# Kernel optimization log

Hardware: AMD Instinct MI355X
Metric: run time of the kernel (lower is better)

## Reference

```python
import jax, jax.numpy as jnp
import numpy as np
import math

H = 16          # n_head
N_EMBD = 1024
EPS = 1e-5      # torch LayerNorm default


def setup_inputs() -> dict:
    key = jax.random.key(0)
    ks = jax.random.split(key, 6)
    B, T, C = 2, 2048, 1024
    x = jax.random.normal(ks[0], (B, T, C), dtype=jnp.float32)
    s = 0.02  # GPT-2 style init scale keeps softmax logits sane
    Wq = jax.random.normal(ks[1], (C, N_EMBD), dtype=jnp.float32) * s
    Wk = jax.random.normal(ks[2], (C, N_EMBD), dtype=jnp.float32) * s
    Wv = jax.random.normal(ks[3], (C, N_EMBD), dtype=jnp.float32) * s
    Wo = jax.random.normal(ks[4], (N_EMBD, C), dtype=jnp.float32) * s
    return {
        "x": x,
        "Wq": Wq, "bq": jnp.zeros((N_EMBD,), jnp.float32),
        "Wk": Wk, "bk": jnp.zeros((N_EMBD,), jnp.float32),
        "Wv": Wv, "bv": jnp.zeros((N_EMBD,), jnp.float32),
        "Wo": Wo, "bo": jnp.zeros((C,), jnp.float32),
        "gamma": jnp.ones((C,), jnp.float32),
        "beta": jnp.zeros((C,), jnp.float32),
    }


def reference(x, Wq, bq, Wk, bk, Wv, bv, Wo, bo, gamma, beta):
    B, T, _ = x.shape
    Dh = N_EMBD // H
    # projections -> (B, H, T, Dh)
    def split_heads(y):
        return y.reshape(B, T, H, Dh).transpose(0, 2, 1, 3)
    q = split_heads(x @ Wq + bq)
    k = split_heads(x @ Wk + bk)
    v = split_heads(x @ Wv + bv)
    # naive causal attention: explicit (B,H,T,T) scores
    att = jnp.einsum("bhtd,bhsd->bhts", q, k) * (1.0 / math.sqrt(Dh))
    causal = jnp.tril(jnp.ones((T, T), dtype=bool))
    att = jnp.where(causal[None, None], att, -jnp.inf)
    att = jax.nn.softmax(att, axis=-1)
    o = jnp.einsum("bhts,bhsd->bhtd", att, v)
    o = o.transpose(0, 2, 1, 3).reshape(B, T, N_EMBD)
    y = o @ Wo + bo
    # LayerNorm (dropout is identity at p=0 / eval)
    mu = jnp.mean(y, axis=-1, keepdims=True)
    var = jnp.var(y, axis=-1, keepdims=True)
    return (y - mu) * jax.lax.rsqrt(var + EPS) * gamma + beta
```

## Files before the change

### kernel.cpp

```cpp
#include <hip/hip_runtime.h>
#include <stdint.h>
#include <stddef.h>

typedef __attribute__((ext_vector_type(8))) short short8;
typedef __attribute__((ext_vector_type(4))) float f32x4;
typedef __attribute__((ext_vector_type(16))) float f32x16;
typedef __attribute__((ext_vector_type(4))) unsigned short us4;
typedef __attribute__((ext_vector_type(4))) unsigned u32x4;

#define DEVI static __device__ __forceinline__

DEVI unsigned short f2bf(float f) {
  unsigned u = __builtin_bit_cast(unsigned, f);
  u += 0x7FFFu + ((u >> 16) & 1u);
  return (unsigned short)(u >> 16);
}

DEVI float bf2f(unsigned short u) {
  return __builtin_bit_cast(float, ((unsigned)u) << 16);
}

DEVI f32x4 mfma16(short8 a, short8 b, f32x4 c) {
  return __builtin_amdgcn_mfma_f32_16x16x32_bf16(a, b, c, 0, 0, 0);
}

DEVI f32x16 mfma32(short8 a, short8 b, f32x16 c) {
  return __builtin_amdgcn_mfma_f32_32x32x16_bf16(a, b, c, 0, 0, 0);
}

DEVI unsigned cvtpk(float lo, float hi) {
  unsigned r;
  asm("v_cvt_pk_bf16_f32 %0, %1, %2" : "=v"(r) : "v"(lo), "v"(hi));
  return r;
}

DEVI void plswap(unsigned& a, unsigned& b) {
  asm("v_permlane32_swap_b32 %0, %1" : "+v"(a), "+v"(b));
}

DEVI float ex2(float x) {
  float r;
  asm("v_exp_f32 %0, %1" : "=v"(r) : "v"(x));
  return r;
}

DEVI float mx3(float a, float b, float c) {
  float r;
  asm("v_max3_f32 %0, %1, %2, %3" : "=v"(r) : "v"(a), "v"(b), "v"(c));
  return r;
}

DEVI f32x16 zero16() {
  f32x16 z;
#pragma unroll
  for (int i = 0; i < 16; ++i) z[i] = 0.f;
  return z;
}

DEVI void glds16(const void* g, void* l) {
  __builtin_amdgcn_global_load_lds(
      (const __attribute__((address_space(1))) void*)g,
      (__attribute__((address_space(3))) void*)l, 16, 0, 0);
}

__global__ __launch_bounds__(256) void k_cvt_x(const float* __restrict__ x,
                                               unsigned short* __restrict__ xb) {
  size_t i = ((size_t)blockIdx.x * 256 + threadIdx.x) * 8;
  f32x4 a = *(const f32x4*)(x + i);
  f32x4 b = *(const f32x4*)(x + i + 4);
  short8 v;
#pragma unroll
  for (int j = 0; j < 4; ++j) {
    v[j] = (short)f2bf(a[j]);
    v[4 + j] = (short)f2bf(b[j]);
  }
  *(short8*)(xb + i) = v;
}

__global__ __launch_bounds__(256) void k_twT4(const float* __restrict__ W0,
                                              const float* __restrict__ W1,
                                              const float* __restrict__ W2,
                                              const float* __restrict__ W3,
                                              unsigned short* __restrict__ WT) {
  __shared__ float tile[64][65];
  const int z = blockIdx.z;
  const float* W = (z == 0) ? W0 : (z == 1) ? W1 : (z == 2) ? W2 : W3;
  unsigned short* out = WT + (size_t)z * 1024 * 1024;
  const int n0 = blockIdx.x * 64, k0 = blockIdx.y * 64;
  const int t = threadIdx.x, rr = t >> 4, cc = (t & 15) * 4;
#pragma unroll
  for (int i = 0; i < 4; ++i) {
    int row = i * 16 + rr;
    f32x4 v = *(const f32x4*)(W + (size_t)(k0 + row) * 1024 + n0 + cc);
#pragma unroll
    for (int j = 0; j < 4; ++j) tile[row][cc + j] = v[j];
  }
  __syncthreads();
#pragma unroll
  for (int i = 0; i < 4; ++i) {
    int nrow = i * 16 + rr;
    us4 u;
#pragma unroll
    for (int j = 0; j < 4; ++j) u[j] = f2bf(tile[cc + j][nrow]);
    *(us4*)(out + (size_t)(n0 + nrow) * 1024 + k0 + cc) = u;
  }
}

template <bool SWAP>
DEVI void gemm_core2(const unsigned short* __restrict__ A,
                     const unsigned short* __restrict__ Bt,
                     int mt, int nt, char* lds, f32x4 (&acc)[4][4]) {
  const int t = threadIdx.x;
  const int l = t & 63, c = l & 15, g = l >> 4;
  const int w = t >> 6, wr = w >> 1, wc = w & 1;
  const int srow = t >> 3;
  const int sxor = (((t & 7) ^ (srow & 7))) * 8;
  const unsigned short* Ab = A + (size_t)(mt * 128 + srow) * 1024 + sxor;
  const unsigned short* Bb = Bt + (size_t)(nt * 128 + srow) * 1024 + sxor;
  const int key = (c & 7);

  auto STAGE = [&](int kt, int buf) {
    char* lb = lds + buf * 32768;
#pragma unroll
    for (int i = 0; i < 4; ++i) {
      glds16(Ab + (size_t)i * 32 * 1024 + kt * 64, lb + i * 4096 + t * 16);
      glds16(Bb + (size_t)i * 32 * 1024 + kt * 64, lb + 16384 + i * 4096 + t * 16);
    }
  };

  STAGE(0, 0);
  asm volatile("s_waitcnt vmcnt(0)" ::: "memory");
  __builtin_amdgcn_s_barrier();
  asm volatile("" ::: "memory");
  for (int kt = 0; kt < 16; ++kt) {
    const int cur = kt & 1;
    if (kt < 15) STAGE(kt + 1, cur ^ 1);
    const char* lb = lds + cur * 32768;
#pragma unroll
    for (int ks = 0; ks < 2; ++ks) {
      short8 af[4], bfr[4];
#pragma unroll
      for (int m = 0; m < 4; ++m)
        af[m] = *(const short8*)(lb + (wr * 64 + m * 16 + c) * 128 +
                                 ((ks * 4 + g) ^ key) * 16);
#pragma unroll
      for (int n = 0; n < 4; ++n)
        bfr[n] = *(const short8*)(lb + 16384 + (wc * 64 + n * 16 + c) * 128 +
                                  ((ks * 4 + g) ^ key) * 16);
#pragma unroll
      for (int m = 0; m < 4; ++m)
#pragma unroll
        for (int n = 0; n < 4; ++n)
          acc[m][n] = SWAP ? mfma16(bfr[n], af[m], acc[m][n])
                           : mfma16(af[m], bfr[n], acc[m][n]);
    }
    asm volatile("s_waitcnt vmcnt(0)" ::: "memory");
    __builtin_amdgcn_s_barrier();
    asm volatile("" ::: "memory");
  }
}

__global__ __launch_bounds__(256) void k_gemm_qkv(
    const unsigned short* __restrict__ A,
    const unsigned short* __restrict__ Wf,
    const float* __restrict__ b0, const float* __restrict__ b1, const float* __restrict__ b2,
    unsigned short* __restrict__ O0, unsigned short* __restrict__ O1,
    unsigned short* __restrict__ O2) {
  __shared__ char lds[65536];
  const int lin = blockIdx.y * 32 + blockIdx.x;
  const int xcd = lin & 7, i = lin >> 3;
  const int ntz = xcd * 3 + (i % 3);
  const int mt = i / 3;
  const int z = ntz >> 3, ntl = ntz & 7;
  const float* bias = (z == 0) ? b0 : (z == 1) ? b1 : b2;
  unsigned short* out = (z == 0) ? O0 : (z == 1) ? O1 : O2;
  f32x4 acc[4][4];
#pragma unroll
  for (int m = 0; m < 4; ++m)
#pragma unroll
    for (int n = 0; n < 4; ++n) acc[m][n] = (f32x4){0.f, 0.f, 0.f, 0.f};
  const int t = threadIdx.x, l = t & 63, c = l & 15, g = l >> 4;
  const int w = t >> 6, wr = w >> 1, wc = w & 1;
  if (z < 2) {
    gemm_core2<true>(A, Wf, mt, ntz, lds, acc);
    const float sc = (z == 0) ? 0.18033688011f : 1.0f;
#pragma unroll
    for (int n = 0; n < 4; ++n) {
      int colb = ntl * 128 + wc * 64 + n * 16 + 4 * g;
      f32x4 bv4 = *(const f32x4*)(bias + colb);
      int h = colb >> 6, d = colb & 63;
#pragma unroll
      for (int m = 0; m < 4; ++m) {
        int rowg = mt * 128 + wr * 64 + m * 16 + c;
        int b = rowg >> 11, tt = rowg & 2047;
        us4 u;
#pragma unroll
        for (int r = 0; r < 4; ++r) u[r] = f2bf((acc[m][n][r] + bv4[r]) * sc);
        *(us4*)(out + ((size_t)(b * 16 + h) * 2048 + tt) * 64 + d) = u;
      }
    }
  } else {
    gemm_core2<false>(A, Wf, mt, ntz, lds, acc);
#pragma unroll
    for (int n = 0; n < 4; ++n) {
      int colg = ntl * 128 + wc * 64 + n * 16 + c;
      float bvv = bias[colg];
      int h = colg >> 6, d = colg & 63;
#pragma unroll
      for (int m = 0; m < 4; ++m) {
        int rowg = mt * 128 + wr * 64 + m * 16 + 4 * g;
        int b = rowg >> 11, tt = rowg & 2047;
        us4 u;
#pragma unroll
        for (int r = 0; r < 4; ++r) u[r] = f2bf(acc[m][n][r] + bvv);
        *(us4*)(out + ((size_t)(b * 16 + h) * 64 + d) * 2048 + tt) = u;
      }
    }
  }
}

__global__ __launch_bounds__(256) void k_gemm_proj(const unsigned short* __restrict__ A,
                                                   const unsigned short* __restrict__ Bt,
                                                   const float* __restrict__ bias,
                                                   float* __restrict__ Y) {
  __shared__ char lds[65536];
  f32x4 acc[4][4];
#pragma unroll
  for (int m = 0; m < 4; ++m)
#pragma unroll
    for (int n = 0; n < 4; ++n) acc[m][n] = (f32x4){0.f, 0.f, 0.f, 0.f};
  const int lin = blockIdx.y * 32 + blockIdx.x;
  const int nt = lin & 7, mt = lin >> 3;
  gemm_core2<true>(A, Bt, mt, nt, lds, acc);
  const int t = threadIdx.x, l = t & 63, c = l & 15, g = l >> 4;
  const int w = t >> 6, wr = w >> 1, wc = w & 1;
#pragma unroll
  for (int n = 0; n < 4; ++n) {
    int colb = nt * 128 + wc * 64 + n * 16 + 4 * g;
    f32x4 bv4 = *(const f32x4*)(bias + colb);
#pragma unroll
    for (int m = 0; m < 4; ++m) {
      int rowg = mt * 128 + wr * 64 + m * 16 + c;
      f32x4 o;
#pragma unroll
      for (int r = 0; r < 4; ++r) o[r] = acc[m][n][r] + bv4[r];
      *(f32x4*)(Y + (size_t)rowg * 1024 + colb) = o;
    }
  }
}

__global__ __launch_bounds__(128) void k_attn5(const unsigned short* __restrict__ Q,
                                               const unsigned short* __restrict__ K,
                                               const unsigned short* __restrict__ VT,
                                               unsigned short* __restrict__ O,
                                               unsigned short* __restrict__ P,
                                               float* __restrict__ ML) {
  __shared__ char lds[32768];
  const int bid = blockIdx.x;
  int qt, c0, nt, mode, bh;
  if (bid < 512) {
    mode = 1; qt = 16 + (bid >> 5); c0 = 0; nt = 16; bh = bid & 31;
  } else {
    int rem = bid - 512;
    int v = 16 - (rem >> 6);
    int sub = rem & 63;
    bh = sub & 31;
    if (sub < 32) { mode = 0; qt = v - 1;  c0 = 0;  nt = v; }
    else          { mode = 2; qt = v + 15; c0 = 16; nt = v; }
  }
  const int t = threadIdx.x;
  const int w = t >> 6, l = t & 63;
  const int lq = l & 31, hi = l >> 5;
  const int q0 = qt * 64 + w * 32;
  const size_t kbase = (size_t)bh * 2048 * 64;
  const size_t vbase = (size_t)bh * 64 * 2048;
  const int srow = t >> 3;
  const int sx = ((t & 7) ^ (srow & 7)) * 8;

  short8 qf[4];
#pragma unroll
  for (int ds = 0; ds < 4; ++ds)
    qf[ds] = *(const short8*)(Q + kbase + (size_t)(q0 + lq) * 64 + 16 * ds + 8 * hi);

  auto STAGE = [&](int ktg, int buf) {
    const unsigned short* Kt = K + kbase + (size_t)ktg * 4096;
    const unsigned short* Vt = VT + vbase + ktg * 64;
    char* lb = lds + buf * 16384;
#pragma unroll
    for (int i = 0; i < 4; ++i) {
      int row = i * 16 + srow;
      glds16(Kt + (size_t)row * 64 + sx, lb + i * 2048 + t * 16);
      glds16(Vt + (size_t)row * 2048 + sx, lb + 8192 + i * 2048 + t * 16);
    }
  };

  f32x16 oacc[2];
  oacc[0] = zero16();
  oacc[1] = zero16();
  float m_s = -1e30f, l_s = 0.f;
  const int rx = lq & 7;

  STAGE(c0, 0);
  for (int kt = 0; kt < nt; ++kt) {
    asm volatile("s_waitcnt vmcnt(0)" ::: "memory");
    __builtin_amdgcn_s_barrier();
    asm volatile("" ::: "memory");
    if (kt + 1 < nt) STAGE(c0 + kt + 1, (kt + 1) & 1);
    const char* lb = lds + (kt & 1) * 16384;
    const int kv0 = (c0 + kt) * 64;
    short8 kf0[4], kf1[4];
#pragma unroll
    for (int ds = 0; ds < 4; ++ds) {
      int blk = ((ds * 2 + hi) ^ rx) * 16;
      kf0[ds] = *(const short8*)(lb + lq * 128 + blk);
      kf1[ds] = *(const short8*)(lb + (lq + 32) * 128 + blk);
    }
    f32x16 st0 = zero16(), st1 = zero16();
    __builtin_amdgcn_s_setprio(1);
#pragma unroll
    for (int ds = 0; ds < 4; ++ds) {
      st0 = mfma32(kf0[ds], qf[ds], st0);
      st1 = mfma32(kf1[ds], qf[ds], st1);
    }
    __builtin_amdgcn_s_setprio(0);
    short8 vf[2][4];
#pragma unroll
    for (int fd = 0; fd < 2; ++fd) {
      int d = fd * 32 + lq;
#pragma unroll
      for (int s = 0; s < 4; ++s)
        vf[fd][s] = *(const short8*)(lb + 8192 + d * 128 + (((s * 2 + hi) ^ rx) * 16));
    }
    if (mode != 1 && kt == nt - 1) {
      const int qg = q0 + lq;
#pragma unroll
      for (int r = 0; r < 16; ++r) {
        int kr = kv0 + (r & 3) + 8 * (r >> 2) + 4 * hi;
        if (kr > qg) st0[r] = -1e30f;
        if (kr + 32 > qg) st1[r] = -1e30f;
      }
    }
    float a8[8];
#pragma unroll
    for (int r = 0; r < 8; ++r)
      a8[r] = fmaxf(mx3(st0[r], st0[r + 8], st1[r]), st1[r + 8]);
    float mxv = mx3(mx3(a8[0], a8[1], a8[2]), mx3(a8[3], a8[4], a8[5]),
                    fmaxf(a8[6], a8[7]));
    if (!__all(mxv - m_s <= 11.5413f)) {
      mxv = fmaxf(mxv, __shfl_xor(mxv, 32, 64));
      float mnew = fmaxf(m_s, mxv);
      float corr = ex2(m_s - mnew);
      m_s = mnew;
      l_s *= corr;
#pragma unroll
      for (int r = 0; r < 16; ++r) {
        oacc[0][r] *= corr;
        oacc[1][r] *= corr;
      }
    }
    unsigned Wp[2][4][2];
    float gs[8];
#pragma unroll
    for (int f = 0; f < 2; ++f)
#pragma unroll
      for (int m4 = 0; m4 < 4; ++m4) {
        float p0 = ex2((f ? st1 : st0)[4 * m4 + 0] - m_s);
        float p1 = ex2((f ? st1 : st0)[4 * m4 + 1] - m_s);
        float p2 = ex2((f ? st1 : st0)[4 * m4 + 2] - m_s);
        float p3 = ex2((f ? st1 : st0)[4 * m4 + 3] - m_s);
        gs[f * 4 + m4] = (p0 + p1) + (p2 + p3);
        Wp[f][m4][0] = cvtpk(p0, p1);
        Wp[f][m4][1] = cvtpk(p2, p3);
      }
    l_s += ((gs[0] + gs[1]) + (gs[2] + gs[3])) + ((gs[4] + gs[5]) + (gs[6] + gs[7]));
    __builtin_amdgcn_s_setprio(1);
#pragma unroll
    for (int s = 0; s < 4; ++s) {
      const int f = s >> 1, s2 = s & 1;
      unsigned a0 = Wp[f][2 * s2][0], b0 = Wp[f][2 * s2 + 1][0];
      unsigned a1 = Wp[f][2 * s2][1], b1 = Wp[f][2 * s2 + 1][1];
      plswap(a0, b0);
      plswap(a1, b1);
      u32x4 pw = {a0, a1, b0, b1};
      short8 pf = __builtin_bit_cast(short8, pw);
      oacc[0] = mfma32(vf[0][s], pf, oacc[0]);
      oacc[1] = mfma32(vf[1][s], pf, oacc[1]);
    }
    __builtin_amdgcn_s_setprio(0);
  }
  l_s += __shfl_xor(l_s, 32, 64);
  if (mode == 0) {
    const float inv = 1.0f / l_s;
    const int b = bh >> 4, h = bh & 15;
    unsigned short* orow = O + ((size_t)b * 2048 + q0 + lq) * 1024 + h * 64 + 4 * hi;
#pragma unroll
    for (int f = 0; f < 2; ++f)
#pragma unroll
      for (int m4 = 0; m4 < 4; ++m4) {
        us4 u;
#pragma unroll
        for (int rr = 0; rr < 4; ++rr) u[rr] = f2bf(oacc[f][4 * m4 + rr] * inv);
        *(us4*)(orow + f * 32 + m4 * 8) = u;
      }
  } else {
    const int pid = ((qt - 16) * 32 + bh) * 2 + (mode - 1);
    unsigned short* prow = P + (size_t)pid * 4096 + (w * 32 + lq) * 64 + 4 * hi;
#pragma unroll
    for (int f = 0; f < 2; ++f)
#pragma unroll
      for (int m4 = 0; m4 < 4; ++m4) {
        us4 u;
#pragma unroll
        for (int rr = 0; rr < 4; ++rr) u[rr] = f2bf(oacc[f][4 * m4 + rr]);
        *(us4*)(prow + f * 32 + m4 * 8) = u;
      }
    if (hi == 0) {
      ML[pid * 128 + w * 32 + lq] = m_s;
      ML[pid * 128 + 64 + w * 32 + lq] = l_s;
    }
  }
}

__global__ __launch_bounds__(64) void k_merge(const unsigned short* __restrict__ P,
                                              const float* __restrict__ ML,
                                              unsigned short* __restrict__ O) {
  const int blk = blockIdx.x;
  const int qt = 16 + (blk >> 5), bh = blk & 31;
  const int pidA = ((qt - 16) * 32 + bh) * 2, pidB = pidA + 1;
  const int r = threadIdx.x;
  float mA = ML[pidA * 128 + r], lA = ML[pidA * 128 + 64 + r];
  float mB = ML[pidB * 128 + r], lB = ML[pidB * 128 + 64 + r];
  float mM = fmaxf(mA, mB);
  float wA = ex2(mA - mM), wB = ex2(mB - mM);
  float inv = 1.f / (lA * wA + lB * wB);
  wA *= inv;
  wB *= inv;
  const unsigned short* pa = P + (size_t)pidA * 4096 + r * 64;
  const unsigned short* pb = P + (size_t)pidB * 4096 + r * 64;
  const int b = bh >> 4, h = bh & 15, q = qt * 64 + r;
  unsigned short* orow = O + ((size_t)b * 2048 + q) * 1024 + h * 64;
#pragma unroll
  for (int j = 0; j < 8; ++j) {
    short8 a = *(const short8*)(pa + j * 8);
    short8 c = *(const short8*)(pb + j * 8);
    short8 o;
#pragma unroll
    for (int k = 0; k < 8; ++k)
      o[k] = (short)f2bf(bf2f((unsigned short)a[k]) * wA +
                         bf2f((unsigned short)c[k]) * wB);
    *(short8*)(orow + j * 8) = o;
  }
}

__global__ __launch_bounds__(256) void k_ln(const float* __restrict__ Y,
                                            const float* __restrict__ gamma,
                                            const float* __restrict__ beta,
                                            float* __restrict__ out) {
  __shared__ float red[8];
  const int row = blockIdx.x, t = threadIdx.x, w = t >> 6, l = t & 63;
  const float* yr = Y + (size_t)row * 1024;
  f32x4 v = *(const f32x4*)(yr + t * 4);
  float s = v[0] + v[1] + v[2] + v[3];
  float ss = v[0] * v[0] + v[1] * v[1] + v[2] * v[2] + v[3] * v[3];
#pragma unroll
  for (int d = 1; d < 64; d <<= 1) {
    s += __shfl_xor(s, d, 64);
    ss += __shfl_xor(ss, d, 64);
  }
  if (l == 0) {
    red[w] = s;
    red[4 + w] = ss;
  }
  __syncthreads();
  s = red[0] + red[1] + red[2] + red[3];
  ss = red[4] + red[5] + red[6] + red[7];
  float mean = s * (1.f / 1024.f);
  float var = ss * (1.f / 1024.f) - mean * mean;
  float rstd = rsqrtf(var + 1e-5f);
  f32x4 gv = *(const f32x4*)(gamma + t * 4);
  f32x4 bv = *(const f32x4*)(beta + t * 4);
  f32x4 ov;
#pragma unroll
  for (int j = 0; j < 4; ++j) ov[j] = (v[j] - mean) * rstd * gv[j] + bv[j];
  *(f32x4*)(out + (size_t)row * 1024 + t * 4) = ov;
}

extern "C" void kernel_launch(void* const* d_in, const int* in_sizes, int n_in,
                              void* d_out, int out_size, void* d_ws, size_t ws_size,
                              hipStream_t stream) {
  (void)in_sizes; (void)n_in; (void)out_size; (void)ws_size;
  const float* x = (const float*)d_in[0];
  const float* Wq = (const float*)d_in[1];
  const float* bq = (const float*)d_in[2];
  const float* Wk = (const float*)d_in[3];
  const float* bk = (const float*)d_in[4];
  const float* Wv = (const float*)d_in[5];
  const float* bv = (const float*)d_in[6];
  const float* Wo = (const float*)d_in[7];
  const float* bo = (const float*)d_in[8];
  const float* gamma = (const float*)d_in[9];
  const float* beta = (const float*)d_in[10];
  char* ws = (char*)d_ws;
  const size_t MB = 1024 * 1024;
  unsigned short* xb = (unsigned short*)(ws);
  unsigned short* WT = (unsigned short*)(ws + 8 * MB);
  unsigned short* WoT = (unsigned short*)(ws + 14 * MB);
  unsigned short* Qb = (unsigned short*)(ws + 16 * MB);
  unsigned short* Kb = (unsigned short*)(ws + 24 * MB);
  unsigned short* VTb = (unsigned short*)(ws + 32 * MB);
  unsigned short* Ob = (unsigned short*)(ws + 40 * MB);
  float* Y = (float*)(ws + 16 * MB);
  unsigned short* Pp = (unsigned short*)(ws);
  float* MLp = (float*)(ws + 8 * MB);

  k_cvt_x<<<2048, 256, 0, stream>>>(x, xb);
  k_twT4<<<dim3(16, 16, 4), 256, 0, stream>>>(Wq, Wk, Wv, Wo, WT);
  k_gemm_qkv<<<dim3(32, 24), 256, 0, stream>>>(xb, WT, bq, bk, bv, Qb, Kb, VTb);
  k_attn5<<<1536, 128, 0, stream>>>(Qb, Kb, VTb, Ob, Pp, MLp);
  k_merge<<<512, 64, 0, stream>>>(Pp, MLp, Ob);
  k_gemm_proj<<<dim3(32, 8), 256, 0, stream>>>(Ob, WoT, bo, Y);
  k_ln<<<4096, 256, 0, stream>>>(Y, gamma, beta, (float*)d_out);
}
```

Before: 118.7 us.

## Use 256x256 tiles with 8 waves and double-buffered LDS in QKV GEMM

Replaces the 128x128, 4-wave QKV projection GEMM with a 256x256 tile computed by 8 waves. It double-buffers 128KB of dynamic LDS so the next K slice loads while the current one is multiplied, and raises wave priority around the MFMA bursts. The aim is more operand reuse per byte loaded and overlap of global loads with compute. In exchange the grid drops to 192 blocks, fewer than the 256 CUs, and the old XCD-aware block remapping is removed. Register pressure also rises with 128 accumulator floats per thread.

```diff
diff --git a/kernel.cpp b/kernel.cpp
--- a/kernel.cpp
+++ b/kernel.cpp
@@ -160,59 +160,122 @@
   }
 }
 
-__global__ __launch_bounds__(256) void k_gemm_qkv(
+template <bool SWAP>
+DEVI void gemm_core3(const unsigned short* __restrict__ A,
+                     const unsigned short* __restrict__ Bt,
+                     int mt, int nt, char* lds, f32x4 (&acc)[8][4]) {
+  const int t = threadIdx.x;
+  const int l = t & 63, c = l & 15, g = l >> 4;
+  const int w = t >> 6, wm = w >> 2, wn = w & 3;
+  const int srow = t >> 3;
+  const int sxor = ((t & 7) ^ (srow & 7)) * 8;
+  const unsigned short* Ab = A + (size_t)(mt * 256 + srow) * 1024 + sxor;
+  const unsigned short* Bb = Bt + (size_t)(nt * 256 + srow) * 1024 + sxor;
+  const int key = c & 7;
+
+  auto STAGE = [&](int kt, int buf) {
+    char* lb = lds + buf * 65536;
+#pragma unroll
+    for (int i = 0; i < 4; ++i) {
+      glds16(Ab + (size_t)(i * 64) * 1024 + kt * 64, lb + i * 8192 + t * 16);
+      glds16(Bb + (size_t)(i * 64) * 1024 + kt * 64, lb + 32768 + i * 8192 + t * 16);
+    }
+  };
+
+  STAGE(0, 0);
+  asm volatile("s_waitcnt vmcnt(0)" ::: "memory");
+  __builtin_amdgcn_s_barrier();
+  asm volatile("" ::: "memory");
+  for (int kt = 0; kt < 16; ++kt) {
+    const int cur = kt & 1;
+    if (kt < 15) STAGE(kt + 1, cur ^ 1);
+    const char* la = lds + cur * 65536;
+    const char* lbB = la + 32768;
+    short8 bf[4][2];
+#pragma unroll
+    for (int fc = 0; fc < 4; ++fc)
+#pragma unroll
+      for (int ks = 0; ks < 2; ++ks) {
+        int brow = wn * 64 + fc * 16 + c;
+        bf[fc][ks] = *(const short8*)(lbB + brow * 128 + (((ks * 4 + g) ^ key) * 16));
+      }
+#pragma unroll
+    for (int p = 0; p < 4; ++p) {
+      short8 af[2][2];
+#pragma unroll
+      for (int r2 = 0; r2 < 2; ++r2)
+#pragma unroll
+        for (int ks = 0; ks < 2; ++ks) {
+          int arow = wm * 128 + (2 * p + r2) * 16 + c;
+          af[r2][ks] = *(const short8*)(la + arow * 128 + (((ks * 4 + g) ^ key) * 16));
+        }
+      __builtin_amdgcn_s_setprio(1);
+#pragma unroll
+      for (int ks = 0; ks < 2; ++ks)
+#pragma unroll
+        for (int r2 = 0; r2 < 2; ++r2)
+#pragma unroll
+          for (int fc = 0; fc < 4; ++fc)
+            acc[2 * p + r2][fc] = SWAP ? mfma16(bf[fc][ks], af[r2][ks], acc[2 * p + r2][fc])
+                                       : mfma16(af[r2][ks], bf[fc][ks], acc[2 * p + r2][fc]);
+      __builtin_amdgcn_s_setprio(0);
+    }
+    asm volatile("s_waitcnt vmcnt(0)" ::: "memory");
+    __builtin_amdgcn_s_barrier();
+    asm volatile("" ::: "memory");
+  }
+}
+
+__global__ __launch_bounds__(512) void k_gemm_qkv2(
     const unsigned short* __restrict__ A,
     const unsigned short* __restrict__ Wf,
     const float* __restrict__ b0, const float* __restrict__ b1, const float* __restrict__ b2,
     unsigned short* __restrict__ O0, unsigned short* __restrict__ O1,
     unsigned short* __restrict__ O2) {
-  __shared__ char lds[65536];
-  const int lin = blockIdx.y * 32 + blockIdx.x;
-  const int xcd = lin & 7, i = lin >> 3;
-  const int ntz = xcd * 3 + (i % 3);
-  const int mt = i / 3;
-  const int z = ntz >> 3, ntl = ntz & 7;
+  extern __shared__ char lds[];
+  const int ntz = blockIdx.x, mt = blockIdx.y;
+  const int z = ntz >> 2, ntl = ntz & 3;
   const float* bias = (z == 0) ? b0 : (z == 1) ? b1 : b2;
   unsigned short* out = (z == 0) ? O0 : (z == 1) ? O1 : O2;
-  f32x4 acc[4][4];
-#pragma unroll
-  for (int m = 0; m < 4; ++m)
+  f32x4 acc[8][4];
+#pragma unroll
+  for (int m = 0; m < 8; ++m)
 #pragma unroll
     for (int n = 0; n < 4; ++n) acc[m][n] = (f32x4){0.f, 0.f, 0.f, 0.f};
   const int t = threadIdx.x, l = t & 63, c = l & 15, g = l >> 4;
-  const int w = t >> 6, wr = w >> 1, wc = w & 1;
+  const int w = t >> 6, wm = w >> 2, wn = w & 3;
   if (z < 2) {
-    gemm_core2<true>(A, Wf, mt, ntz, lds, acc);
+    gemm_core3<true>(A, Wf, mt, ntz, lds, acc);
     const float sc = (z == 0) ? 0.18033688011f : 1.0f;
 #pragma unroll
-    for (int n = 0; n < 4; ++n) {
-      int colb = ntl * 128 + wc * 64 + n * 16 + 4 * g;
+    for (int fc = 0; fc < 4; ++fc) {
+      int colb = ntl * 256 + wn * 64 + fc * 16 + 4 * g;
       f32x4 bv4 = *(const f32x4*)(bias + colb);
       int h = colb >> 6, d = colb & 63;
 #pragma unroll
-      for (int m = 0; m < 4; ++m) {
-        int rowg = mt * 128 + wr * 64 + m * 16 + c;
+      for (int fr = 0; fr < 8; ++fr) {
+        int rowg = mt * 256 + wm * 128 + fr * 16 + c;
         int b = rowg >> 11, tt = rowg & 2047;
         us4 u;
 #pragma unroll
-        for (int r = 0; r < 4; ++r) u[r] = f2bf((acc[m][n][r] + bv4[r]) * sc);
+        for (int r = 0; r < 4; ++r) u[r] = f2bf((acc[fr][fc][r] + bv4[r]) * sc);
         *(us4*)(out + ((size_t)(b * 16 + h) * 2048 + tt) * 64 + d) = u;
       }
     }
   } else {
-    gemm_core2<false>(A, Wf, mt, ntz, lds, acc);
-#pragma unroll
-    for (int n = 0; n < 4; ++n) {
-      int colg = ntl * 128 + wc * 64 + n * 16 + c;
+    gemm_core3<false>(A, Wf, mt, ntz, lds, acc);
+#pragma unroll
+    for (int fc = 0; fc < 4; ++fc) {
+      int colg = ntl * 256 + wn * 64 + fc * 16 + c;
       float bvv = bias[colg];
       int h = colg >> 6, d = colg & 63;
 #pragma unroll
-      for (int m = 0; m < 4; ++m) {
-        int rowg = mt * 128 + wr * 64 + m * 16 + 4 * g;
+      for (int fr = 0; fr < 8; ++fr) {
+        int rowg = mt * 256 + wm * 128 + fr * 16 + 4 * g;
         int b = rowg >> 11, tt = rowg & 2047;
         us4 u;
 #pragma unroll
-        for (int r = 0; r < 4; ++r) u[r] = f2bf(acc[m][n][r] + bvv);
+        for (int r = 0; r < 4; ++r) u[r] = f2bf(acc[fr][fc][r] + bvv);
         *(us4*)(out + ((size_t)(b * 16 + h) * 64 + d) * 2048 + tt) = u;
       }
     }
@@ -515,7 +578,7 @@
 
   k_cvt_x<<<2048, 256, 0, stream>>>(x, xb);
   k_twT4<<<dim3(16, 16, 4), 256, 0, stream>>>(Wq, Wk, Wv, Wo, WT);
-  k_gemm_qkv<<<dim3(32, 24), 256, 0, stream>>>(xb, WT, bq, bk, bv, Qb, Kb, VTb);
+  k_gemm_qkv2<<<dim3(12, 16), 512, 131072, stream>>>(xb, WT, bq, bk, bv, Qb, Kb, VTb);
   k_attn5<<<1536, 128, 0, stream>>>(Qb, Kb, VTb, Ob, Pp, MLp);
   k_merge<<<512, 64, 0, stream>>>(Pp, MLp, Ob);
   k_gemm_proj<<<dim3(32, 8), 256, 0, stream>>>(Ob, WoT, bo, Y);
```

After: 115.8 us. -2.5%, faster.
